# Performance work log

Measured on AMD Instinct MI355X. Metric: run time of the kernel, lower is better.

## Reference

```python
import jax, jax.numpy as jnp
import numpy as np

# Static dims (from init_kwargs / input_specs)
B, D, H, W, T, C = 1, 16, 32, 32, 4, 128
G, NH = 4, 8
HD = C // NH
NW = (D // G) * (H // G) * (W // G)   # windows per sample
N = G ** 3 * T                         # tokens per window (T-major ordering)
MLP_H = 4 * C
SCALE = 1.0 / float(np.sqrt(HD))
EPS = 1e-5


def _ln(x, g, b):
    m = x.mean(-1, keepdims=True)
    v = ((x - m) ** 2).mean(-1, keepdims=True)
    return (x - m) / jnp.sqrt(v + EPS) * g + b


def setup_inputs() -> dict:
    key = jax.random.key(0)
    ks = jax.random.split(key, 10)
    s = 0.02
    return {
        "x": jax.random.normal(ks[0], (B, D, H, W, T, C), jnp.float32),
        "norm1_g": jnp.ones((C,), jnp.float32),
        "norm1_b": jnp.zeros((C,), jnp.float32),
        "pos_embed": jax.random.normal(ks[1], (G, G, G, C), jnp.float32) * s,
        "time_embed": jax.random.normal(ks[2], (T, 1, 1, 1, C), jnp.float32) * s,
        "qkv_w": jax.random.normal(ks[3], (3 * C, C), jnp.float32) * s,
        "qkv_b": jnp.zeros((3 * C,), jnp.float32),
        "proj_w": jax.random.normal(ks[4], (C, C), jnp.float32) * s,
        "proj_b": jnp.zeros((C,), jnp.float32),
        "conv_w": jax.random.normal(ks[5], (C, 1, 3, 3, 3), jnp.float32) * s,  # depthwise
        "conv_b": jnp.zeros((C,), jnp.float32),
        "exln_g": jnp.ones((C,), jnp.float32),
        "exln_b": jnp.zeros((C,), jnp.float32),
        "norm2_g": jnp.ones((C,), jnp.float32),
        "norm2_b": jnp.zeros((C,), jnp.float32),
        "fc1_w": jax.random.normal(ks[6], (MLP_H, C), jnp.float32) * s,
        "fc1_b": jnp.zeros((MLP_H,), jnp.float32),
        "fc2_w": jax.random.normal(ks[7], (C, MLP_H), jnp.float32) * s,
        "fc2_b": jnp.zeros((C,), jnp.float32),
    }


def reference(x, norm1_g, norm1_b, pos_embed, time_embed, qkv_w, qkv_b,
              proj_w, proj_b, conv_w, conv_b, exln_g, exln_b,
              norm2_g, norm2_b, fc1_w, fc1_b, fc2_w, fc2_b):
    # --- window partition (lsda_flag=0, local SDA; dims divisible by G -> padding=0) ---
    xw = x.reshape(B, D // G, G, H // G, G, W // G, G, T, C)
    xw = xw.transpose(0, 1, 3, 5, 7, 2, 4, 6, 8)   # (B, Dg, Hg, Wg, T, G, G, G, C)
    xw = xw.reshape(B * NW, N, C)                   # token dim is T-major over (T,G,G,G)

    # --- pre-norm + window attention ---
    h = _ln(xw, norm1_g, norm1_b)
    h = h.reshape(B * NW, T, G, G, G, C)
    h = (h + pos_embed + time_embed).reshape(B * NW, N, C)  # learned spatial + temporal PE
    qkv = (h @ qkv_w.T + qkv_b).reshape(B * NW, N, 3, NH, HD).transpose(2, 0, 3, 1, 4)
    q, k, v = qkv[0] * SCALE, qkv[1], qkv[2]        # (B_, NH, N, HD)
    attn = jax.nn.softmax(jnp.einsum('bhnd,bhmd->bhnm', q, k), axis=-1)
    o = jnp.einsum('bhnm,bhmd->bhnd', attn, v).transpose(0, 2, 1, 3).reshape(B * NW, N, C)
    o = o @ proj_w.T + proj_b

    # --- window merge (inverse of partition) ---
    y = o.reshape(B, D // G, H // G, W // G, T, G, G, G, C)
    y = y.transpose(0, 1, 5, 2, 6, 3, 7, 4, 8).reshape(B, D, H, W, T, C)

    # --- depthwise 3x3x3 Conv3d over (D,H,W), T folded into batch, then LN ---
    xc = y.transpose(0, 4, 5, 1, 2, 3).reshape(B * T, C, D, H, W)
    xc = jax.lax.conv_general_dilated(
        xc, conv_w, window_strides=(1, 1, 1),
        padding=((1, 1), (1, 1), (1, 1)),
        feature_group_count=C,
        dimension_numbers=('NCDHW', 'OIDHW', 'NCDHW'))
    xc = xc + conv_b[None, :, None, None, None]
    y = xc.reshape(B, T, C, D, H, W).transpose(0, 3, 4, 5, 1, 2)
    y = _ln(y, exln_g, exln_b)

    # --- MLP with residual: x = mlp(norm2(x)) + x ---
    h2 = _ln(y, norm2_g, norm2_b)
    h2 = jax.nn.gelu(h2 @ fc1_w.T + fc1_b, approximate=False)
    h2 = h2 @ fc2_w.T + fc2_b
    return h2 + y
```

## Files before the change

kernel.cpp:

```cpp
#include <hip/hip_runtime.h>
#include <hip/hip_bf16.h>


typedef __attribute__((ext_vector_type(8))) short  s16x8;
typedef __attribute__((ext_vector_type(4))) short  s16x4;
typedef __attribute__((ext_vector_type(4))) float  f32x4;

#define CC    128
#define NWIN  256
#define NTOK  256
#define TOKS  65536
#define SCALE 0.25f
#define LNEPS 1e-5f

__device__ __forceinline__ float b2f(short s) {
  union { unsigned u; float f; } c; c.u = ((unsigned)(unsigned short)s) << 16; return c.f;
}
__device__ __forceinline__ short f2b(float f) {
  __hip_bfloat16 h = __float2bfloat16(f);
  return *reinterpret_cast<short*>(&h);
}
__device__ __forceinline__ float fast_gelu(float x) {
  float u = 1.595769122f * x * fmaf(0.044715f, x*x, 1.0f);
  return x / (1.0f + __expf(-u));
}

__device__ __forceinline__ f32x4 mfma16x16x16_bf16(s16x4 a, s16x4 b, f32x4 c) {
#if __has_builtin(__builtin_amdgcn_mfma_f32_16x16x16_bf16)
  return __builtin_amdgcn_mfma_f32_16x16x16_bf16(a, b, c, 0, 0, 0);
#elif __has_builtin(__builtin_amdgcn_mfma_f32_16x16x16bf16_1k)
  return __builtin_amdgcn_mfma_f32_16x16x16bf16_1k(a, b, c, 0, 0, 0);
#else
  f32x4 d;
  asm("v_mfma_f32_16x16x16_bf16 %0, %1, %2, %3" : "=v"(d) : "v"(a), "v"(b), "v"(c));
  return d;
#endif
}

__global__ void prep_kernel(const float* __restrict__ qkv_w, const float* __restrict__ proj_w,
                            const float* __restrict__ fc1_w, const float* __restrict__ fc2_w,
                            const float* __restrict__ conv_w,
                            __hip_bfloat16* wq, __hip_bfloat16* wp,
                            __hip_bfloat16* w1, __hip_bfloat16* w2, float* cwT) {
  int idx = blockIdx.x * 256 + threadIdx.x;
  if (idx < 49152) {
    wq[idx] = __float2bfloat16(qkv_w[idx]);
  } else if (idx < 65536) {
    wp[idx - 49152] = __float2bfloat16(proj_w[idx - 49152]);
  } else if (idx < 131072) {
    w1[idx - 65536] = __float2bfloat16(fc1_w[idx - 65536]);
  } else if (idx < 196608) {
    w2[idx - 131072] = __float2bfloat16(fc2_w[idx - 131072]);
  } else if (idx < 196608 + 27*128) {
    int j = idx - 196608;
    int tap = j >> 7, c = j & 127;
    cwT[tap*128 + c] = conv_w[c*27 + tap];
  }
}

__global__ __launch_bounds__(256) void ln1_pe_kernel(
    const float* __restrict__ x, const float* __restrict__ g, const float* __restrict__ b,
    const float* __restrict__ pos, const float* __restrict__ te,
    __hip_bfloat16* __restrict__ hb) {
  int wv = threadIdx.x >> 6, lane = threadIdx.x & 63;
  int tk = blockIdx.x * 4 + wv;
  int wid = tk >> 8, n = tk & 255;
  int t = n >> 6, gd = (n >> 4) & 3, gh = (n >> 2) & 3, gw = n & 3;
  int wd = wid >> 6, wh = (wid >> 3) & 7, ww = wid & 7;
  int d = wd*4 + gd, h = wh*4 + gh, w = ww*4 + gw;
  size_t xoff = ((size_t)((d*32 + h)*32 + w)*4 + t) * CC;
  float v0 = x[xoff + lane], v1 = x[xoff + lane + 64];
  float s = v0 + v1, sq = v0*v0 + v1*v1;
  for (int m = 32; m; m >>= 1) { s += __shfl_xor(s, m); sq += __shfl_xor(sq, m); }
  float mean = s * (1.f/128.f);
  float var  = sq * (1.f/128.f) - mean*mean;
  float rstd = rsqrtf(var + LNEPS);
  int pb = ((gd*4 + gh)*4 + gw) * CC, tb = t * CC;
  float h0 = (v0 - mean)*rstd*g[lane]    + b[lane]    + pos[pb + lane]    + te[tb + lane];
  float h1 = (v1 - mean)*rstd*g[lane+64] + b[lane+64] + pos[pb + lane+64] + te[tb + lane+64];
  hb[(size_t)tk*CC + lane]      = __float2bfloat16(h0);
  hb[(size_t)tk*CC + lane + 64] = __float2bfloat16(h1);
}

template <int MODE, int KK>
__global__ __launch_bounds__(256) void gemm_kernel(
    const short* __restrict__ Ag, const short* __restrict__ Wg,
    const float* __restrict__ bias,
    void* __restrict__ out0, const float* __restrict__ resid) {
  __shared__ __align__(16) short As[128*72];
  __shared__ __align__(16) short Bs[128*72];
  const int tid = threadIdx.x;
  const int m0 = blockIdx.x * 128;
  const int n0 = blockIdx.y * 128;
  const int lane = tid & 63, wv = tid >> 6;
  const int wr = wv >> 1, wc = wv & 1;
  const int fr = lane & 15, kg = lane >> 4;

  f32x4 acc[4][4];
#pragma unroll
  for (int i = 0; i < 4; ++i)
#pragma unroll
    for (int j = 0; j < 4; ++j) acc[i][j] = (f32x4)0.f;

#pragma unroll
  for (int kc = 0; kc < KK; kc += 64) {
    __syncthreads();
#pragma unroll
    for (int i = 0; i < 4; ++i) {
      int c = tid + i*256;
      int row = c >> 3, col8 = (c & 7) * 8;
      s16x8 va = *(const s16x8*)(Ag + (size_t)(m0 + row)*KK + kc + col8);
      s16x8 vb = *(const s16x8*)(Wg + (size_t)(n0 + row)*KK + kc + col8);
      *(s16x8*)&As[row*72 + col8] = va;
      *(s16x8*)&Bs[row*72 + col8] = vb;
    }
    __syncthreads();
#pragma unroll
    for (int ks = 0; ks < 2; ++ks) {
      s16x8 a[4], b[4];
#pragma unroll
      for (int i = 0; i < 4; ++i)
        a[i] = *(const s16x8*)&As[(wr*64 + i*16 + fr)*72 + ks*32 + kg*8];
#pragma unroll
      for (int j = 0; j < 4; ++j)
        b[j] = *(const s16x8*)&Bs[(wc*64 + j*16 + fr)*72 + ks*32 + kg*8];
#pragma unroll
      for (int i = 0; i < 4; ++i)
#pragma unroll
        for (int j = 0; j < 4; ++j)
          acc[i][j] = __builtin_amdgcn_mfma_f32_16x16x32_bf16(b[j], a[i], acc[i][j], 0, 0, 0);
    }
  }

  const int nbb = n0 + wc*64 + kg*4;
  f32x4 bj4[4];
#pragma unroll
  for (int j = 0; j < 4; ++j) bj4[j] = *(const f32x4*)&bias[nbb + j*16];

#pragma unroll
  for (int i = 0; i < 4; ++i) {
    const int m = m0 + wr*64 + i*16 + fr;
    if constexpr (MODE == 0) {
      short* qs = (short*)out0;
      const int sec = n0 >> 7;
      const float scl = (sec == 0) ? SCALE : 1.0f;
      const int wid = m >> 8, ntok = m & 255;
      const int rowbase = sec*8388608 + (wid*8)*4096 + ntok*16 + (nbb & 15);
#pragma unroll
      for (int j = 0; j < 4; ++j) {
        const int head = ((nbb + j*16) >> 4) & 7;
        f32x4 v = acc[i][j];
        s16x4 o;
        o[0] = f2b(fmaf(v[0], scl, bj4[j].x*scl));
        o[1] = f2b(fmaf(v[1], scl, bj4[j].y*scl));
        o[2] = f2b(fmaf(v[2], scl, bj4[j].z*scl));
        o[3] = f2b(fmaf(v[3], scl, bj4[j].w*scl));
        *(s16x4*)&qs[rowbase + head*4096] = o;
      }
    } else if constexpr (MODE == 1) {
      short* y1o = (short*)out0;
      const int wid = m >> 8, ntok = m & 255;
      const int t = ntok >> 6, gd = (ntok >> 4) & 3, gh = (ntok >> 2) & 3, gw = ntok & 3;
      const int wd = wid >> 6, wh = (wid >> 3) & 7, ww = wid & 7;
      const int sr = (((wd*4 + gd)*32 + wh*4 + gh)*32 + ww*4 + gw)*4 + t;
      const int base = sr*CC + nbb;
#pragma unroll
      for (int j = 0; j < 4; ++j) {
        f32x4 v = acc[i][j];
        s16x4 o;
        o[0] = f2b(v[0] + bj4[j].x); o[1] = f2b(v[1] + bj4[j].y);
        o[2] = f2b(v[2] + bj4[j].z); o[3] = f2b(v[3] + bj4[j].w);
        *(s16x4*)&y1o[base + j*16] = o;
      }
    } else if constexpr (MODE == 2) {
      short* gp = (short*)out0;
      const int base = m*512 + nbb;
#pragma unroll
      for (int j = 0; j < 4; ++j) {
        f32x4 v = acc[i][j];
        s16x4 o;
        o[0] = f2b(fast_gelu(v[0] + bj4[j].x)); o[1] = f2b(fast_gelu(v[1] + bj4[j].y));
        o[2] = f2b(fast_gelu(v[2] + bj4[j].z)); o[3] = f2b(fast_gelu(v[3] + bj4[j].w));
        *(s16x4*)&gp[base + j*16] = o;
      }
    } else {
      float* outp = (float*)out0;
      const int base = m*CC + nbb;
#pragma unroll
      for (int j = 0; j < 4; ++j) {
        f32x4 v = acc[i][j];
        f32x4 rz = *(const f32x4*)&resid[base + j*16];
        f32x4 o;
        o.x = v[0] + bj4[j].x + rz.x; o.y = v[1] + bj4[j].y + rz.y;
        o.z = v[2] + bj4[j].z + rz.z; o.w = v[3] + bj4[j].w + rz.w;
        *(f32x4*)&outp[base + j*16] = o;
      }
    }
  }
}

#define KPAD 20
#define VPAD 264
__global__ __launch_bounds__(256) void attn_mfma_kernel(
    const __hip_bfloat16* __restrict__ qb, const __hip_bfloat16* __restrict__ kb,
    const __hip_bfloat16* __restrict__ vb, __hip_bfloat16* __restrict__ ob) {
  __shared__ __align__(16) short kL[256*KPAD];
  __shared__ __align__(16) short vT[16*VPAD];
  const int bh = blockIdx.x;
  const int wid = bh >> 3, head = bh & 7;
  const int tid = threadIdx.x;
  const short* kg = (const short*)kb + (size_t)bh*4096;
  const short* vg = (const short*)vb + (size_t)bh*4096;
  const short* qg = (const short*)qb + (size_t)bh*4096;
  {
    s16x8 a0 = *(const s16x8*)&kg[tid*16];
    s16x8 a1 = *(const s16x8*)&kg[tid*16 + 8];
    *(s16x8*)&kL[tid*KPAD]     = a0;
    *(s16x8*)&kL[tid*KPAD + 8] = a1;
    s16x8 b0 = *(const s16x8*)&vg[tid*16];
    s16x8 b1 = *(const s16x8*)&vg[tid*16 + 8];
#pragma unroll
    for (int d = 0; d < 8; ++d) {
      vT[d*VPAD + tid]     = b0[d];
      vT[(d+8)*VPAD + tid] = b1[d];
    }
  }
  __syncthreads();
  const int wv = tid >> 6, lane = tid & 63;
  const int fr = lane & 15, hi = lane >> 4;
  s16x4 kfrag[16], vfrag[16];
#pragma unroll
  for (int t = 0; t < 16; ++t) {
    kfrag[t] = *(const s16x4*)&kL[(t*16 + fr)*KPAD + hi*4];
    vfrag[t] = *(const s16x4*)&vT[fr*VPAD + t*16 + hi*4];
  }
  short* obs = (short*)ob;
  for (int qt = 0; qt < 4; ++qt) {
    const int q0 = wv*64 + qt*16;
    s16x4 qfrag = *(const s16x4*)&qg[(q0 + fr)*16 + hi*4];
    f32x4 st[16];
#pragma unroll
    for (int kt = 0; kt < 16; ++kt)
      st[kt] = mfma16x16x16_bf16(kfrag[kt], qfrag, (f32x4)0.f);
    float den = 0.f;
    f32x4 oacc = (f32x4)0.f;
#pragma unroll
    for (int kt = 0; kt < 16; ++kt) {
      float e0 = __expf(st[kt][0]), e1 = __expf(st[kt][1]);
      float e2 = __expf(st[kt][2]), e3 = __expf(st[kt][3]);
      den += (e0 + e1) + (e2 + e3);
      s16x4 pa;
      pa[0] = f2b(e0); pa[1] = f2b(e1); pa[2] = f2b(e2); pa[3] = f2b(e3);
      oacc = mfma16x16x16_bf16(vfrag[kt], pa, oacc);
    }
    den += __shfl_xor(den, 16);
    den += __shfl_xor(den, 32);
    float inv = 1.f / den;
    s16x4 ov;
    ov[0] = f2b(oacc[0]*inv); ov[1] = f2b(oacc[1]*inv);
    ov[2] = f2b(oacc[2]*inv); ov[3] = f2b(oacc[3]*inv);
    *(s16x4*)&obs[((size_t)wid*256 + q0 + fr)*CC + head*16 + hi*4] = ov;
  }
}

__global__ __launch_bounds__(256) void conv_ln_kernel(
    const __hip_bfloat16* __restrict__ y1b, const float* __restrict__ wT,
    const float* __restrict__ cb,
    const float* __restrict__ exg, const float* __restrict__ exb,
    const float* __restrict__ n2g, const float* __restrict__ n2b,
    float* __restrict__ yb, __hip_bfloat16* __restrict__ h2) {
  const int tid = threadIdx.x;
  const int sp = blockIdx.x*8 + (tid >> 5);
  const int cbase = (tid & 31) * 4;
  const int w = sp & 31, h = (sp >> 5) & 31, d = sp >> 10;
  const short* ys = (const short*)y1b;

  f32x4 bias = *(const f32x4*)&cb[cbase];
  f32x4 acc0 = bias, acc1 = bias, acc2 = bias, acc3 = bias;

#pragma unroll
  for (int dd = -1; dd <= 1; ++dd) {
    int dn = d + dd; if ((unsigned)dn >= 16u) continue;
#pragma unroll
    for (int dh = -1; dh <= 1; ++dh) {
      int hn = h + dh; if ((unsigned)hn >= 32u) continue;
#pragma unroll
      for (int dw = -1; dw <= 1; ++dw) {
        int wn = w + dw; if ((unsigned)wn >= 32u) continue;
        int tap = ((dd+1)*3 + (dh+1))*3 + (dw+1);
        f32x4 wv = *(const f32x4*)&wT[tap*CC + cbase];
        const short* base = &ys[(size_t)(((dn*32 + hn)*32 + wn)*4)*CC + cbase];
        s16x4 v0 = *(const s16x4*)(base);
        s16x4 v1 = *(const s16x4*)(base + CC);
        s16x4 v2 = *(const s16x4*)(base + 2*CC);
        s16x4 v3 = *(const s16x4*)(base + 3*CC);
        acc0.x = fmaf(b2f(v0[0]), wv.x, acc0.x); acc0.y = fmaf(b2f(v0[1]), wv.y, acc0.y);
        acc0.z = fmaf(b2f(v0[2]), wv.z, acc0.z); acc0.w = fmaf(b2f(v0[3]), wv.w, acc0.w);
        acc1.x = fmaf(b2f(v1[0]), wv.x, acc1.x); acc1.y = fmaf(b2f(v1[1]), wv.y, acc1.y);
        acc1.z = fmaf(b2f(v1[2]), wv.z, acc1.z); acc1.w = fmaf(b2f(v1[3]), wv.w, acc1.w);
        acc2.x = fmaf(b2f(v2[0]), wv.x, acc2.x); acc2.y = fmaf(b2f(v2[1]), wv.y, acc2.y);
        acc2.z = fmaf(b2f(v2[2]), wv.z, acc2.z); acc2.w = fmaf(b2f(v2[3]), wv.w, acc2.w);
        acc3.x = fmaf(b2f(v3[0]), wv.x, acc3.x); acc3.y = fmaf(b2f(v3[1]), wv.y, acc3.y);
        acc3.z = fmaf(b2f(v3[2]), wv.z, acc3.z); acc3.w = fmaf(b2f(v3[3]), wv.w, acc3.w);
      }
    }
  }

  f32x4 eg = *(const f32x4*)&exg[cbase];
  f32x4 eb = *(const f32x4*)&exb[cbase];
  f32x4 ng = *(const f32x4*)&n2g[cbase];
  f32x4 nb = *(const f32x4*)&n2b[cbase];

  f32x4 accs[4] = {acc0, acc1, acc2, acc3};
#pragma unroll
  for (int t = 0; t < 4; ++t) {
    f32x4 a = accs[t];
    float s  = (a.x + a.y) + (a.z + a.w);
    float sq = (a.x*a.x + a.y*a.y) + (a.z*a.z + a.w*a.w);
#pragma unroll
    for (int m = 1; m <= 16; m <<= 1) { s += __shfl_xor(s, m); sq += __shfl_xor(sq, m); }
    float mean = s * (1.f/128.f);
    float var  = sq * (1.f/128.f) - mean*mean;
    float rstd = rsqrtf(var + LNEPS);
    f32x4 y;
    y.x = (a.x - mean)*rstd*eg.x + eb.x;
    y.y = (a.y - mean)*rstd*eg.y + eb.y;
    y.z = (a.z - mean)*rstd*eg.z + eb.z;
    y.w = (a.w - mean)*rstd*eg.w + eb.w;
    *(f32x4*)&yb[(size_t)(sp*4 + t)*CC + cbase] = y;
    float s2  = (y.x + y.y) + (y.z + y.w);
    float sq2 = (y.x*y.x + y.y*y.y) + (y.z*y.z + y.w*y.w);
#pragma unroll
    for (int m = 1; m <= 16; m <<= 1) { s2 += __shfl_xor(s2, m); sq2 += __shfl_xor(sq2, m); }
    float mean2 = s2 * (1.f/128.f);
    float var2  = sq2 * (1.f/128.f) - mean2*mean2;
    float rstd2 = rsqrtf(var2 + LNEPS);
    s16x4 hb;
    hb[0] = f2b((y.x - mean2)*rstd2*ng.x + nb.x);
    hb[1] = f2b((y.y - mean2)*rstd2*ng.y + nb.y);
    hb[2] = f2b((y.z - mean2)*rstd2*ng.z + nb.z);
    hb[3] = f2b((y.w - mean2)*rstd2*ng.w + nb.w);
    *(s16x4*)&((short*)h2)[(size_t)(sp*4 + t)*CC + cbase] = hb;
  }
}

extern "C" void kernel_launch(void* const* d_in, const int* in_sizes, int n_in,
                              void* d_out, int out_size, void* d_ws, size_t ws_size,
                              hipStream_t stream) {
  const float* x      = (const float*)d_in[0];
  const float* n1g    = (const float*)d_in[1];
  const float* n1b    = (const float*)d_in[2];
  const float* pos    = (const float*)d_in[3];
  const float* te     = (const float*)d_in[4];
  const float* qkv_w  = (const float*)d_in[5];
  const float* qkv_b  = (const float*)d_in[6];
  const float* proj_w = (const float*)d_in[7];
  const float* proj_b = (const float*)d_in[8];
  const float* conv_w = (const float*)d_in[9];
  const float* conv_b = (const float*)d_in[10];
  const float* exg    = (const float*)d_in[11];
  const float* exb    = (const float*)d_in[12];
  const float* n2g    = (const float*)d_in[13];
  const float* n2b    = (const float*)d_in[14];
  const float* fc1_w  = (const float*)d_in[15];
  const float* fc1_b  = (const float*)d_in[16];
  const float* fc2_w  = (const float*)d_in[17];
  const float* fc2_b  = (const float*)d_in[18];

  char* wsb = (char*)d_ws;
  __hip_bfloat16* wq  = (__hip_bfloat16*)(wsb);
  __hip_bfloat16* wp  = (__hip_bfloat16*)(wsb + 98304);
  __hip_bfloat16* w1  = (__hip_bfloat16*)(wsb + 131072);
  __hip_bfloat16* w2  = (__hip_bfloat16*)(wsb + 262144);
  float*          cwT = (float*)(wsb + 393216);

  const size_t A_OFF = (size_t)1 << 20;
  const size_t B_OFF = A_OFF + ((size_t)16 << 20);
  const size_t C_OFF = B_OFF + ((size_t)48 << 20);

  __hip_bfloat16* hbuf = (__hip_bfloat16*)(wsb + A_OFF);
  __hip_bfloat16* obuf = (__hip_bfloat16*)(wsb + A_OFF);
  __hip_bfloat16* h2in = (__hip_bfloat16*)(wsb + A_OFF);
  __hip_bfloat16* qkvb = (__hip_bfloat16*)(wsb + B_OFF);
  __hip_bfloat16* qb   = qkvb;
  __hip_bfloat16* kb   = qkvb + 8388608;
  __hip_bfloat16* vb   = qkvb + 16777216;
  __hip_bfloat16* y1   = (__hip_bfloat16*)(wsb + B_OFF);
  float* yb   = (float*)(wsb + B_OFF + ((size_t)16 << 20));
  __hip_bfloat16* gbuf = (__hip_bfloat16*)(wsb + C_OFF);

  prep_kernel<<<782, 256, 0, stream>>>(qkv_w, proj_w, fc1_w, fc2_w, conv_w,
                                       wq, wp, w1, w2, cwT);
  ln1_pe_kernel<<<TOKS/4, 256, 0, stream>>>(x, n1g, n1b, pos, te, hbuf);
  gemm_kernel<0, 128><<<dim3(TOKS/128, 3), 256, 0, stream>>>(
      (const short*)hbuf, (const short*)wq, qkv_b, (void*)qkvb, nullptr);
  attn_mfma_kernel<<<NWIN*8, 256, 0, stream>>>(qb, kb, vb, obuf);
  gemm_kernel<1, 128><<<dim3(TOKS/128, 1), 256, 0, stream>>>(
      (const short*)obuf, (const short*)wp, proj_b, (void*)y1, nullptr);
  conv_ln_kernel<<<16384/8, 256, 0, stream>>>(y1, cwT, conv_b,
      exg, exb, n2g, n2b, yb, h2in);
  gemm_kernel<2, 128><<<dim3(TOKS/128, 4), 256, 0, stream>>>(
      (const short*)h2in, (const short*)w1, fc1_b, (void*)gbuf, nullptr);
  gemm_kernel<3, 512><<<dim3(TOKS/128, 1), 256, 0, stream>>>(
      (const short*)gbuf, (const short*)w2, fc2_b, (void*)d_out, yb);
}
```

Measured before the change: 179.3 us.

## Pad conv input with zero halo, widen conv lanes, store residual as fp16

The proj GEMM now writes its output into a zero-padded (18x34x34) spatial buffer, which is cleared by a memset each call. This lets the depthwise conv kernel drop its boundary checks. The conv kernel also uses 16 threads per site with 8 channels each and 16-byte loads. The post-LN residual y is stored as fp16 instead of fp32, which halves its write and its reread in the final GEMM but adds rounding error on the residual path. The extra memset of roughly 20 MB adds traffic and one more launch.

```diff
diff --git a/kernel.cpp b/kernel.cpp
--- a/kernel.cpp
+++ b/kernel.cpp
@@ -5,13 +5,19 @@
 typedef __attribute__((ext_vector_type(8))) short  s16x8;
 typedef __attribute__((ext_vector_type(4))) short  s16x4;
 typedef __attribute__((ext_vector_type(4))) float  f32x4;
+typedef __attribute__((ext_vector_type(8))) _Float16 f16x8;
+typedef __attribute__((ext_vector_type(4))) _Float16 f16x4;
 
 #define CC    128
 #define NWIN  256
-#define NTOK  256
 #define TOKS  65536
 #define SCALE 0.25f
 #define LNEPS 1e-5f
+#define PD 18
+#define PH 34
+#define PW 34
+#define PSITES (PD*PH*PW)
+#define Y1P_SHORTS ((size_t)PSITES*512)
 
 __device__ __forceinline__ float b2f(short s) {
   union { unsigned u; float f; } c; c.u = ((unsigned)(unsigned short)s) << 16; return c.f;
@@ -86,7 +92,7 @@
 __global__ __launch_bounds__(256) void gemm_kernel(
     const short* __restrict__ Ag, const short* __restrict__ Wg,
     const float* __restrict__ bias,
-    void* __restrict__ out0, const float* __restrict__ resid) {
+    void* __restrict__ out0, const _Float16* __restrict__ resid) {
   __shared__ __align__(16) short As[128*72];
   __shared__ __align__(16) short Bs[128*72];
   const int tid = threadIdx.x;
@@ -162,7 +168,7 @@
       const int wid = m >> 8, ntok = m & 255;
       const int t = ntok >> 6, gd = (ntok >> 4) & 3, gh = (ntok >> 2) & 3, gw = ntok & 3;
       const int wd = wid >> 6, wh = (wid >> 3) & 7, ww = wid & 7;
-      const int sr = (((wd*4 + gd)*32 + wh*4 + gh)*32 + ww*4 + gw)*4 + t;
+      const int sr = (((wd*4 + gd + 1)*PH + wh*4 + gh + 1)*PW + ww*4 + gw + 1)*4 + t;
       const int base = sr*CC + nbb;
 #pragma unroll
       for (int j = 0; j < 4; ++j) {
@@ -189,10 +195,10 @@
 #pragma unroll
       for (int j = 0; j < 4; ++j) {
         f32x4 v = acc[i][j];
-        f32x4 rz = *(const f32x4*)&resid[base + j*16];
+        f16x4 rz = *(const f16x4*)&resid[base + j*16];
         f32x4 o;
-        o.x = v[0] + bj4[j].x + rz.x; o.y = v[1] + bj4[j].y + rz.y;
-        o.z = v[2] + bj4[j].z + rz.z; o.w = v[3] + bj4[j].w + rz.w;
+        o.x = v[0] + bj4[j].x + (float)rz[0]; o.y = v[1] + bj4[j].y + (float)rz[1];
+        o.z = v[2] + bj4[j].z + (float)rz[2]; o.w = v[3] + bj4[j].w + (float)rz[3];
         *(f32x4*)&outp[base + j*16] = o;
       }
     }
@@ -264,83 +270,93 @@
 }
 
 __global__ __launch_bounds__(256) void conv_ln_kernel(
-    const __hip_bfloat16* __restrict__ y1b, const float* __restrict__ wT,
+    const __hip_bfloat16* __restrict__ y1p, const float* __restrict__ wT,
     const float* __restrict__ cb,
     const float* __restrict__ exg, const float* __restrict__ exb,
     const float* __restrict__ n2g, const float* __restrict__ n2b,
-    float* __restrict__ yb, __hip_bfloat16* __restrict__ h2) {
+    _Float16* __restrict__ yb, __hip_bfloat16* __restrict__ h2) {
   const int tid = threadIdx.x;
-  const int sp = blockIdx.x*8 + (tid >> 5);
-  const int cbase = (tid & 31) * 4;
+  const int sp = blockIdx.x*16 + (tid >> 4);
+  const int cbase = (tid & 15) * 8;
   const int w = sp & 31, h = (sp >> 5) & 31, d = sp >> 10;
-  const short* ys = (const short*)y1b;
-
-  f32x4 bias = *(const f32x4*)&cb[cbase];
-  f32x4 acc0 = bias, acc1 = bias, acc2 = bias, acc3 = bias;
-
-#pragma unroll
-  for (int dd = -1; dd <= 1; ++dd) {
-    int dn = d + dd; if ((unsigned)dn >= 16u) continue;
-#pragma unroll
-    for (int dh = -1; dh <= 1; ++dh) {
-      int hn = h + dh; if ((unsigned)hn >= 32u) continue;
+  const int psite = ((d+1)*PH + (h+1))*PW + (w+1);
+  const short* base = (const short*)y1p + (size_t)psite*512 + cbase;
+
+  float acc[4][8];
+  {
+    f32x4 cb0 = *(const f32x4*)&cb[cbase];
+    f32x4 cb1 = *(const f32x4*)&cb[cbase + 4];
+#pragma unroll
+    for (int t = 0; t < 4; ++t) {
+      acc[t][0]=cb0.x; acc[t][1]=cb0.y; acc[t][2]=cb0.z; acc[t][3]=cb0.w;
+      acc[t][4]=cb1.x; acc[t][5]=cb1.y; acc[t][6]=cb1.z; acc[t][7]=cb1.w;
+    }
+  }
+
+#pragma unroll
+  for (int dd = -1; dd <= 1; ++dd)
+#pragma unroll
+    for (int dh = -1; dh <= 1; ++dh)
 #pragma unroll
       for (int dw = -1; dw <= 1; ++dw) {
-        int wn = w + dw; if ((unsigned)wn >= 32u) continue;
-        int tap = ((dd+1)*3 + (dh+1))*3 + (dw+1);
-        f32x4 wv = *(const f32x4*)&wT[tap*CC + cbase];
-        const short* base = &ys[(size_t)(((dn*32 + hn)*32 + wn)*4)*CC + cbase];
-        s16x4 v0 = *(const s16x4*)(base);
-        s16x4 v1 = *(const s16x4*)(base + CC);
-        s16x4 v2 = *(const s16x4*)(base + 2*CC);
-        s16x4 v3 = *(const s16x4*)(base + 3*CC);
-        acc0.x = fmaf(b2f(v0[0]), wv.x, acc0.x); acc0.y = fmaf(b2f(v0[1]), wv.y, acc0.y);
-        acc0.z = fmaf(b2f(v0[2]), wv.z, acc0.z); acc0.w = fmaf(b2f(v0[3]), wv.w, acc0.w);
-        acc1.x = fmaf(b2f(v1[0]), wv.x, acc1.x); acc1.y = fmaf(b2f(v1[1]), wv.y, acc1.y);
-        acc1.z = fmaf(b2f(v1[2]), wv.z, acc1.z); acc1.w = fmaf(b2f(v1[3]), wv.w, acc1.w);
-        acc2.x = fmaf(b2f(v2[0]), wv.x, acc2.x); acc2.y = fmaf(b2f(v2[1]), wv.y, acc2.y);
-        acc2.z = fmaf(b2f(v2[2]), wv.z, acc2.z); acc2.w = fmaf(b2f(v2[3]), wv.w, acc2.w);
-        acc3.x = fmaf(b2f(v3[0]), wv.x, acc3.x); acc3.y = fmaf(b2f(v3[1]), wv.y, acc3.y);
-        acc3.z = fmaf(b2f(v3[2]), wv.z, acc3.z); acc3.w = fmaf(b2f(v3[3]), wv.w, acc3.w);
+        const int tap = ((dd+1)*3 + (dh+1))*3 + (dw+1);
+        const int toff = ((dd*PH + dh)*PW + dw)*512;
+        f32x4 w0 = *(const f32x4*)&wT[tap*CC + cbase];
+        f32x4 w1 = *(const f32x4*)&wT[tap*CC + cbase + 4];
+#pragma unroll
+        for (int t = 0; t < 4; ++t) {
+          s16x8 v = *(const s16x8*)(base + toff + t*CC);
+          acc[t][0] = fmaf(b2f(v[0]), w0.x, acc[t][0]);
+          acc[t][1] = fmaf(b2f(v[1]), w0.y, acc[t][1]);
+          acc[t][2] = fmaf(b2f(v[2]), w0.z, acc[t][2]);
+          acc[t][3] = fmaf(b2f(v[3]), w0.w, acc[t][3]);
+          acc[t][4] = fmaf(b2f(v[4]), w1.x, acc[t][4]);
+          acc[t][5] = fmaf(b2f(v[5]), w1.y, acc[t][5]);
+          acc[t][6] = fmaf(b2f(v[6]), w1.z, acc[t][6]);
+          acc[t][7] = fmaf(b2f(v[7]), w1.w, acc[t][7]);
+        }
       }
-    }
-  }
-
-  f32x4 eg = *(const f32x4*)&exg[cbase];
-  f32x4 eb = *(const f32x4*)&exb[cbase];
-  f32x4 ng = *(const f32x4*)&n2g[cbase];
-  f32x4 nb = *(const f32x4*)&n2b[cbase];
-
-  f32x4 accs[4] = {acc0, acc1, acc2, acc3};
+
+  f32x4 eg0 = *(const f32x4*)&exg[cbase], eg1 = *(const f32x4*)&exg[cbase+4];
+  f32x4 eb0 = *(const f32x4*)&exb[cbase], eb1 = *(const f32x4*)&exb[cbase+4];
+  f32x4 ng0 = *(const f32x4*)&n2g[cbase], ng1 = *(const f32x4*)&n2g[cbase+4];
+  f32x4 nb0 = *(const f32x4*)&n2b[cbase], nb1 = *(const f32x4*)&n2b[cbase+4];
+  float eg[8] = {eg0.x,eg0.y,eg0.z,eg0.w,eg1.x,eg1.y,eg1.z,eg1.w};
+  float eb[8] = {eb0.x,eb0.y,eb0.z,eb0.w,eb1.x,eb1.y,eb1.z,eb1.w};
+  float ng[8] = {ng0.x,ng0.y,ng0.z,ng0.w,ng1.x,ng1.y,ng1.z,ng1.w};
+  float nb[8] = {nb0.x,nb0.y,nb0.z,nb0.w,nb1.x,nb1.y,nb1.z,nb1.w};
+
 #pragma unroll
   for (int t = 0; t < 4; ++t) {
-    f32x4 a = accs[t];
-    float s  = (a.x + a.y) + (a.z + a.w);
-    float sq = (a.x*a.x + a.y*a.y) + (a.z*a.z + a.w*a.w);
-#pragma unroll
-    for (int m = 1; m <= 16; m <<= 1) { s += __shfl_xor(s, m); sq += __shfl_xor(sq, m); }
+    float s = 0.f, sq = 0.f;
+#pragma unroll
+    for (int c = 0; c < 8; ++c) { s += acc[t][c]; sq = fmaf(acc[t][c], acc[t][c], sq); }
+#pragma unroll
+    for (int m = 1; m <= 8; m <<= 1) { s += __shfl_xor(s, m); sq += __shfl_xor(sq, m); }
     float mean = s * (1.f/128.f);
     float var  = sq * (1.f/128.f) - mean*mean;
     float rstd = rsqrtf(var + LNEPS);
-    f32x4 y;
-    y.x = (a.x - mean)*rstd*eg.x + eb.x;
-    y.y = (a.y - mean)*rstd*eg.y + eb.y;
-    y.z = (a.z - mean)*rstd*eg.z + eb.z;
-    y.w = (a.w - mean)*rstd*eg.w + eb.w;
-    *(f32x4*)&yb[(size_t)(sp*4 + t)*CC + cbase] = y;
-    float s2  = (y.x + y.y) + (y.z + y.w);
-    float sq2 = (y.x*y.x + y.y*y.y) + (y.z*y.z + y.w*y.w);
-#pragma unroll
-    for (int m = 1; m <= 16; m <<= 1) { s2 += __shfl_xor(s2, m); sq2 += __shfl_xor(sq2, m); }
+    float y[8];
+    f16x8 yo;
+#pragma unroll
+    for (int c = 0; c < 8; ++c) {
+      y[c] = (acc[t][c] - mean)*rstd*eg[c] + eb[c];
+      yo[c] = (_Float16)y[c];
+    }
+    *(f16x8*)&yb[(size_t)(sp*4 + t)*CC + cbase] = yo;
+    float s2 = 0.f, sq2 = 0.f;
+#pragma unroll
+    for (int c = 0; c < 8; ++c) { s2 += y[c]; sq2 = fmaf(y[c], y[c], sq2); }
+#pragma unroll
+    for (int m = 1; m <= 8; m <<= 1) { s2 += __shfl_xor(s2, m); sq2 += __shfl_xor(sq2, m); }
     float mean2 = s2 * (1.f/128.f);
     float var2  = sq2 * (1.f/128.f) - mean2*mean2;
     float rstd2 = rsqrtf(var2 + LNEPS);
-    s16x4 hb;
-    hb[0] = f2b((y.x - mean2)*rstd2*ng.x + nb.x);
-    hb[1] = f2b((y.y - mean2)*rstd2*ng.y + nb.y);
-    hb[2] = f2b((y.z - mean2)*rstd2*ng.z + nb.z);
-    hb[3] = f2b((y.w - mean2)*rstd2*ng.w + nb.w);
-    *(s16x4*)&((short*)h2)[(size_t)(sp*4 + t)*CC + cbase] = hb;
+    s16x8 ho;
+#pragma unroll
+    for (int c = 0; c < 8; ++c)
+      ho[c] = f2b((y[c] - mean2)*rstd2*ng[c] + nb[c]);
+    *(s16x8*)&((short*)h2)[(size_t)(sp*4 + t)*CC + cbase] = ho;
   }
 }
 
@@ -385,8 +401,8 @@
   __hip_bfloat16* qb   = qkvb;
   __hip_bfloat16* kb   = qkvb + 8388608;
   __hip_bfloat16* vb   = qkvb + 16777216;
-  __hip_bfloat16* y1   = (__hip_bfloat16*)(wsb + B_OFF);
-  float* yb   = (float*)(wsb + B_OFF + ((size_t)16 << 20));
+  __hip_bfloat16* y1p  = (__hip_bfloat16*)(wsb + B_OFF);
+  _Float16* yb = (_Float16*)(wsb + B_OFF + ((size_t)24 << 20));
   __hip_bfloat16* gbuf = (__hip_bfloat16*)(wsb + C_OFF);
 
   prep_kernel<<<782, 256, 0, stream>>>(qkv_w, proj_w, fc1_w, fc2_w, conv_w,
@@ -395,9 +411,10 @@
   gemm_kernel<0, 128><<<dim3(TOKS/128, 3), 256, 0, stream>>>(
       (const short*)hbuf, (const short*)wq, qkv_b, (void*)qkvb, nullptr);
   attn_mfma_kernel<<<NWIN*8, 256, 0, stream>>>(qb, kb, vb, obuf);
+  hipMemsetAsync((void*)y1p, 0, Y1P_SHORTS*sizeof(short), stream);
   gemm_kernel<1, 128><<<dim3(TOKS/128, 1), 256, 0, stream>>>(
-      (const short*)obuf, (const short*)wp, proj_b, (void*)y1, nullptr);
-  conv_ln_kernel<<<16384/8, 256, 0, stream>>>(y1, cwT, conv_b,
+      (const short*)obuf, (const short*)wp, proj_b, (void*)y1p, nullptr);
+  conv_ln_kernel<<<16384/16, 256, 0, stream>>>(y1p, cwT, conv_b,
       exg, exb, n2g, n2b, yb, h2in);
   gemm_kernel<2, 128><<<dim3(TOKS/128, 4), 256, 0, stream>>>(
       (const short*)h2in, (const short*)w1, fc1_b, (void*)gbuf, nullptr);
```

Measured after the change: 183.0 us. 2.1% more time.
